# Kernel optimization log

Measured on AMD Instinct MI355X. Metric: run time of the kernel, lower is better.

Reference implementation:

```python
import jax, jax.numpy as jnp
import numpy as np

B, N, K = 4, 1024, 20
DM, DI, DS, DC, DR = 1024, 2048, 16, 4, 64
BITS, GRID = 10, 0.02
BINS = (1, 2, 4, 8, 16, 32)


def _lrelu(x):
    return jnp.where(x >= 0, x, 0.2 * x)


def _bn(x, w, b, m, v, eps=1e-5):
    return (x - m) * (w * jax.lax.rsqrt(v + eps)) + b


def _ln(x, w, b, eps=1e-5):
    mu = jnp.mean(x, -1, keepdims=True)
    var = jnp.mean((x - mu) ** 2, -1, keepdims=True)
    return (x - mu) * jax.lax.rsqrt(var + eps) * w + b


def _knn(x, k):
    # x: (B,N,C) -> (B,N,k) indices of k nearest (largest neg sq dist)
    xx = jnp.sum(x * x, -1)
    d = 2 * jnp.einsum('bnc,bmc->bnm', x, x) - xx[:, :, None] - xx[:, None, :]
    return jax.lax.top_k(d, k)[1]


def _edge_conv(x, w, bw, bb, bm, bv, k):
    idx = _knn(x, k)
    nb = jax.vmap(lambda f, i: f[i])(x, idx)            # (B,N,k,C) row gather
    ctr = jnp.broadcast_to(x[:, :, None, :], nb.shape)
    feat = jnp.concatenate([nb - ctr, ctr], -1)         # (B,N,k,2C)
    h = _lrelu(_bn(jnp.einsum('bnkc,oc->bnko', feat, w), bw, bb, bm, bv))
    return jnp.max(h, axis=2)                           # (B,N,O)


def _hilbert(g):
    # Skilling's AxesToTranspose, 3D, BITS bits/axis. g: (...,3) int32 -> (...,) int32
    xs = [g[..., i] for i in range(3)]
    Q = 1 << (BITS - 1)
    while Q > 1:
        P = Q - 1
        for i in range(3):
            cond = (xs[i] & Q) != 0
            if i == 0:
                xs[0] = jnp.where(cond, xs[0] ^ P, xs[0])
            else:
                t = (xs[0] ^ xs[i]) & P
                n0 = jnp.where(cond, xs[0] ^ P, xs[0] ^ t)
                ni = jnp.where(cond, xs[i], xs[i] ^ t)
                xs[0], xs[i] = n0, ni
        Q >>= 1
    for i in range(1, 3):
        xs[i] = xs[i] ^ xs[i - 1]
    t = jnp.zeros_like(xs[0])
    Q = 1 << (BITS - 1)
    while Q > 1:
        t = jnp.where((xs[2] & Q) != 0, t ^ (Q - 1), t)
        Q >>= 1
    xs = [v ^ t for v in xs]
    code = jnp.zeros_like(xs[0])
    for bit in range(BITS - 1, -1, -1):
        for i in range(3):
            code = (code << 1) | ((xs[i] >> bit) & 1)
    return code


def _serial_order(pts, trans):
    g = jnp.floor(pts / GRID).astype(jnp.int32)
    g = g - jnp.min(g, axis=1, keepdims=True)
    g = jnp.clip(g, 0, (1 << BITS) - 1)
    if trans:
        g = g[..., jnp.array([1, 0, 2])]
    return jnp.argsort(_hilbert(g), axis=1)             # per-batch serialization order


def _take(f, o):
    return jnp.take_along_axis(f, o[..., None], axis=1)


def _mamba(x, in_w, conv_w, conv_b, xproj_w, dt_w, dt_b, A_log, Dp, out_w):
    Bm, L, _ = x.shape
    xc, z = jnp.split(x @ in_w.T, 2, axis=-1)           # (B,L,DI) each
    xp = jnp.pad(xc, ((0, 0), (DC - 1, 0), (0, 0)))     # causal depthwise conv
    xc = sum(conv_w[:, j] * xp[:, j:j + L, :] for j in range(DC)) + conv_b
    xc = jax.nn.silu(xc)
    xdbl = xc @ xproj_w.T
    dt, Bs, Cs = jnp.split(xdbl, [DR, DR + DS], axis=-1)
    dt = jax.nn.softplus(dt @ dt_w.T + dt_b)            # (B,L,DI)
    A = -jnp.exp(A_log)                                 # (DI,DS)

    def step(h, inp):
        dt_t, B_t, C_t, u_t = inp
        h = h * jnp.exp(dt_t[..., None] * A) + (dt_t * u_t)[..., None] * B_t[:, None, :]
        return h, jnp.einsum('bdn,bn->bd', h, C_t)

    tm = lambda a: jnp.moveaxis(a, 1, 0)
    h0 = jnp.zeros((Bm, DI, DS), x.dtype)
    _, ys = jax.lax.scan(step, h0, (tm(dt), tm(Bs), tm(Cs), tm(xc)))
    y = jnp.moveaxis(ys, 0, 1) + xc * Dp
    return (y * jax.nn.silu(z)) @ out_w.T


def _forward(x, c1_w, bn1_w, bn1_b, bn1_m, bn1_v, c2_w, bn2_w, bn2_b, bn2_m, bn2_v,
             c3_w, bn3_w, bn3_b, bn3_m, bn3_v, c4_w, bn4_w, bn4_b, bn4_m, bn4_v,
             c5_w, bn5_w, bn5_b, bn5_m, bn5_v, pe1_w, pe1_b, pe2_w, pe2_b,
             gamma, beta, blkn_w, blkn_b, in_w, conv_w, conv_b, xproj_w,
             dt_w, dt_b, A_log, D, out_w, normf_w, normf_b, ft_w, ft_b):
    pts = jnp.transpose(x, (0, 2, 1))                   # (B,N,3)
    x1 = _edge_conv(pts, c1_w, bn1_w, bn1_b, bn1_m, bn1_v, K)
    x2 = _edge_conv(x1, c2_w, bn2_w, bn2_b, bn2_m, bn2_v, K)
    x3 = _edge_conv(x2, c3_w, bn3_w, bn3_b, bn3_m, bn3_v, K)
    x4 = _edge_conv(x3, c4_w, bn4_w, bn4_b, bn4_m, bn4_v, K)
    dg = _lrelu(_bn(jnp.einsum('bnc,oc->bno', jnp.concatenate([x1, x2, x3, x4], -1), c5_w),
                    bn5_w, bn5_b, bn5_m, bn5_v))        # (B,N,1024)
    pos5 = jax.nn.gelu(pts @ pe1_w.T + pe1_b, approximate=False) @ pe2_w.T + pe2_b
    of = _serial_order(pts, False)
    ob = _serial_order(pts, True)
    xs = jnp.concatenate([_take(dg, of) * gamma + beta,
                          _take(dg, ob) * gamma + beta], 1)   # (B,2N,1024)
    ps = jnp.concatenate([_take(pos5, of), _take(pos5, ob)], 1)
    hs = xs + ps
    hs = hs + _mamba(_ln(hs, blkn_w, blkn_b), in_w, conv_w, conv_b, xproj_w,
                     dt_w, dt_b, A_log, D, out_w)
    hs = _ln(hs, normf_w, normf_b)
    x_all = jnp.concatenate([hs, dg], axis=1)           # (B,3N,1024)
    P = x_all.shape[1]
    feats = []
    for nbin in BINS:
        zz = x_all.reshape(B, nbin, P // nbin, DM)
        feats.append(jnp.mean(zz, 2) + jnp.max(zz, 2))
    bf = jnp.transpose(jnp.concatenate(feats, 1), (1, 0, 2))  # (63,B,1024)
    return bf @ ft_w.T + ft_b                           # (63,B,256)


def setup_inputs() -> dict:
    ks = iter(jax.random.split(jax.random.key(0), 80))
    f32 = jnp.float32
    def nrm(shape, s):
        return jax.random.normal(next(ks), shape, f32) * s
    d = {}
    d['x'] = jax.random.normal(next(ks), (B, 3, N), f32)
    for name, (o, i) in dict(c1=(64, 6), c2=(64, 128), c3=(128, 128),
                             c4=(256, 256), c5=(1024, 512)).items():
        d[name + '_w'] = nrm((o, i), 1.0 / np.sqrt(i))
    for name, c in dict(bn1=64, bn2=64, bn3=128, bn4=256, bn5=1024).items():
        d[name + '_w'] = 1.0 + nrm((c,), 0.05)
        d[name + '_b'] = nrm((c,), 0.05)
        d[name + '_m'] = nrm((c,), 0.05)
        d[name + '_v'] = 1.0 + 0.1 * jax.random.uniform(next(ks), (c,), f32)
    d['pe1_w'] = nrm((DM // 2, 3), 1.0 / np.sqrt(3))
    d['pe1_b'] = nrm((DM // 2,), 0.02)
    d['pe2_w'] = nrm((DM, DM // 2), 1.0 / np.sqrt(DM // 2))
    d['pe2_b'] = nrm((DM,), 0.02)
    d['gamma'] = 1.0 + nrm((DM,), 0.02)
    d['beta'] = nrm((DM,), 0.02)
    d['blkn_w'] = jnp.ones((DM,), f32)
    d['blkn_b'] = jnp.zeros((DM,), f32)
    d['in_w'] = nrm((2 * DI, DM), 1.0 / np.sqrt(DM))
    d['conv_w'] = nrm((DI, DC), 1.0 / np.sqrt(DC))
    d['conv_b'] = jnp.zeros((DI,), f32)
    d['xproj_w'] = nrm((DR + 2 * DS, DI), 1.0 / np.sqrt(DI))
    d['dt_w'] = nrm((DI, DR), DR ** -0.5)
    dt = jnp.exp(jax.random.uniform(next(ks), (DI,), f32) * np.log(0.1 / 1e-3) + np.log(1e-3))
    d['dt_b'] = dt + jnp.log(-jnp.expm1(-dt))           # inverse softplus
    d['A_log'] = jnp.log(jnp.broadcast_to(jnp.arange(1, DS + 1, dtype=f32), (DI, DS)))
    d['D'] = jnp.ones((DI,), f32)
    d['out_w'] = nrm((DM, DI), 1.0 / np.sqrt(DI))
    d['normf_w'] = jnp.ones((DM,), f32)
    d['normf_b'] = jnp.zeros((DM,), f32)
    d['ft_w'] = nrm((256, DM), 1.0 / np.sqrt(DM))
    d['ft_b'] = jnp.zeros((256,), f32)
    return d


def reference(x, c1_w, bn1_w, bn1_b, bn1_m, bn1_v, c2_w, bn2_w, bn2_b, bn2_m, bn2_v,
              c3_w, bn3_w, bn3_b, bn3_m, bn3_v, c4_w, bn4_w, bn4_b, bn4_m, bn4_v,
              c5_w, bn5_w, bn5_b, bn5_m, bn5_v, pe1_w, pe1_b, pe2_w, pe2_b,
              gamma, beta, blkn_w, blkn_b, in_w, conv_w, conv_b, xproj_w,
              dt_w, dt_b, A_log, D, out_w, normf_w, normf_b, ft_w, ft_b):
    return _forward(x, c1_w, bn1_w, bn1_b, bn1_m, bn1_v, c2_w, bn2_w, bn2_b, bn2_m, bn2_v,
                    c3_w, bn3_w, bn3_b, bn3_m, bn3_v, c4_w, bn4_w, bn4_b, bn4_m, bn4_v,
                    c5_w, bn5_w, bn5_b, bn5_m, bn5_v, pe1_w, pe1_b, pe2_w, pe2_b,
                    gamma, beta, blkn_w, blkn_b, in_w, conv_w, conv_b, xproj_w,
                    dt_w, dt_b, A_log, D, out_w, normf_w, normf_b, ft_w, ft_b)
```

## Files before the change

kernel.cpp:

```cpp
#include <hip/hip_runtime.h>
#include <hip/hip_bf16.h>
#include <cstdint>
#include <cstddef>

static constexpr int BB = 4, NN = 1024;
static constexpr int DM = 1024, DI = 2048, DSN = 16, DCN = 4;
static constexpr int LL = 2048, PP = 3072;

typedef unsigned short u16;
typedef __bf16 bfv8 __attribute__((ext_vector_type(8)));
typedef float fv4 __attribute__((ext_vector_type(4)));

__device__ __forceinline__ u16 f2bf(float f) {
  unsigned u = __float_as_uint(f);
  return (u16)((u + 0x7FFFu + ((u >> 16) & 1u)) >> 16);
}
__device__ __forceinline__ float bf2f(u16 h) { return __uint_as_float(((unsigned)h) << 16); }

__device__ __forceinline__ void gload_lds16(const void* g, void* l) {
  __builtin_amdgcn_global_load_lds((const __attribute__((address_space(1))) void*)g,
                                   (__attribute__((address_space(3))) void*)l, 16, 0, 0);
}

__global__ __launch_bounds__(256) void k_fill(unsigned* __restrict__ p, unsigned n32, unsigned pat) {
// ... 93 lines not shown
#pragma unroll
    for (int kk = 0; kk < 16; ++kk) {
      float a[4], bv[4];
#pragma unroll
      for (int i = 0; i < 4; ++i) a[i] = As[kk][(trow << 2) + i];
#pragma unroll
      for (int j = 0; j < 4; ++j) bv[j] = Bs[kk][(tcol << 2) + j];
#pragma unroll
      for (int i = 0; i < 4; ++i)
#pragma unroll
        for (int j = 0; j < 4; ++j) acc[i][j] += a[i] * bv[j];
    }
    __syncthreads();
  }

#pragma unroll
  for (int i = 0; i < 4; ++i) {
    int gm = m0 + (trow << 2) + i;
#pragma unroll
    for (int j = 0; j < 4; ++j) {
      int gn = n0 + (tcol << 2) + j;
      float v = 2.f * acc[i][j] - xx[(b << 10) + gm] - xx[(b << 10) + gn];
      D[((size_t)(b << 10) + gm) * 1024 + gn] = v;
    }
  }
}

__global__ __launch_bounds__(256) void k_sel(const float* __restrict__ D, int* __restrict__ idxo) {
  const int wv = threadIdx.x >> 6, lane = threadIdx.x & 63;
  const int row = (blockIdx.x << 2) + wv;
  const float* dr = D + (size_t)row * 1024;
  float4 c0 = *(const float4*)(dr + (lane << 2));
  float4 c1 = *(const float4*)(dr + 256 + (lane << 2));
  float4 c2 = *(const float4*)(dr + 512 + (lane << 2));
  float4 c3 = *(const float4*)(dr + 768 + (lane << 2));
  float v[16] = {c0.x, c0.y, c0.z, c0.w, c1.x, c1.y, c1.z, c1.w,
                 c2.x, c2.y, c2.z, c2.w, c3.x, c3.y, c3.z, c3.w};
  const int gbase = lane << 2;
  for (int t = 0; t < 20; ++t) {
    float bv = v[0];
    int bi = gbase;
#pragma unroll
    for (int r = 1; r < 16; ++r) {
      int gi = ((r >> 2) << 8) + gbase + (r & 3);
      if (v[r] > bv) { bv = v[r]; bi = gi; }
    }
#pragma unroll
    for (int o = 32; o; o >>= 1) {
      float ov = __shfl_down(bv, o);
      int oi = __shfl_down(bi, o);
      if (ov > bv || (ov == bv && oi < bi)) { bv = ov; bi = oi; }
    }
    bi = __shfl(bi, 0);
    if (lane == 0) idxo[row * 20 + t] = bi;
#pragma unroll
    for (int r = 0; r < 16; ++r) {
      int gi = ((r >> 2) << 8) + gbase + (r & 3);
      if (gi == bi) v[r] = -3e38f;
    }
  }
}

template <int O>
__global__ __launch_bounds__(256) void k_edge_max(const float* __restrict__ G, const float* __restrict__ base,
                                                  const int* __restrict__ idxi,
                                                  const float* __restrict__ bw, const float* __restrict__ bbp,
                                                  const float* __restrict__ bm, const float* __restrict__ bvv,
                                                  float* __restrict__ out, int ldo) {
  __shared__ int ids[20];
  const int rn = blockIdx.x;
  const int tid = threadIdx.x;
  if (tid < 20) ids[tid] = idxi[rn * 20 + tid];
  __syncthreads();
  const int b = rn >> 10;
  float mx = -3e38f, mn = 3e38f;
#pragma unroll 5
  for (int k = 0; k < 20; ++k) {
    float v = G[((size_t)(b << 10) + ids[k]) * O + tid];
    mx = fmaxf(mx, v); mn = fminf(mn, v);
  }
  float s = bw[tid] * rsqrtf(bvv[tid] + 1e-5f);
  float red = (s >= 0.f) ? mx : mn;
  float v = (base[(size_t)rn * O + tid] + red - bm[tid]) * s + bbp[tid];
  out[(size_t)rn * ldo + tid] = (v >= 0.f) ? v : 0.2f * v;
}

template <int EPI>
__global__ __launch_bounds__(256) void k_gemm(const float* __restrict__ A, int lda,
                                              const float* __restrict__ Bm, int ldb, int boff, int bdiff,
                                              float* __restrict__ C, int ldc, int M, int N, int Kd,
                                              const float* __restrict__ p1) {
  __shared__ float As[16][68];
  __shared__ float Bs[16][68];
  const int tid = threadIdx.x;
  const int m0 = blockIdx.y << 6, n0 = blockIdx.x << 6;
  const int tcol = tid & 15, trow = tid >> 4;
  float acc[4][4];
#pragma unroll
  for (int i = 0; i < 4; ++i)
#pragma unroll
    for (int j = 0; j < 4; ++j) acc[i][j] = 0.f;

  for (int k0 = 0; k0 < Kd; k0 += 16) {
#pragma unroll
    for (int p = 0; p < 4; ++p) {
      int lin = tid + (p << 8);
      int r = lin >> 4, kk = lin & 15;
      int gk = k0 + kk;
      int gm = m0 + r;
      As[kk][r] = (gm < M && gk < Kd) ? A[(size_t)gm * lda + gk] : 0.f;
      int gn = n0 + r;
      float bv = 0.f;
      if (gn < N && gk < Kd) {
        bv = Bm[(size_t)gn * ldb + gk + boff];
        if (bdiff) bv -= Bm[(size_t)gn * ldb + gk];
      }
      Bs[kk][r] = bv;
    }
    __syncthreads();
#pragma unroll
    for (int kk = 0; kk < 16; ++kk) {
      float a[4], bv[4];
#pragma unroll
      for (int i = 0; i < 4; ++i) a[i] = As[kk][(trow << 2) + i];
#pragma unroll
      for (int j = 0; j < 4; ++j) bv[j] = Bs[kk][(tcol << 2) + j];
#pragma unroll
      for (int i = 0; i < 4; ++i)
#pragma unroll
        for (int j = 0; j < 4; ++j) acc[i][j] += a[i] * bv[j];
    }
    __syncthreads();
  }

#pragma unroll
  for (int i = 0; i < 4; ++i) {
    int gm = m0 + (trow << 2) + i;
    if (gm >= M) continue;
#pragma unroll
    for (int j = 0; j < 4; ++j) {
      int gn = n0 + (tcol << 2) + j;
      if (gn >= N) continue;
      float v = acc[i][j];
      if (EPI == 2) {
        v += p1[gn];
        v = 0.5f * v * (1.f + erff(v * 0.70710678118654752440f));
      }
      C[(size_t)gm * ldc + gn] = v;
    }
  }
}

template <int EPI>
__global__ __launch_bounds__(256) void k_mgemm(const u16* __restrict__ A, const u16* __restrict__ W,
                                               float* __restrict__ C, int ldc, int M, int N, int K, int alda,
                                               const float* __restrict__ p1, const float* __restrict__ p2,
                                               const float* __restrict__ p3, const float* __restrict__ p4,
                                               u16* __restrict__ obf, void* outp, const void* modesrc) {
  __shared__ u16 Asl[2][4096];
  __shared__ u16 Bsl[2][4096];
  const int tid = threadIdx.x;
  const int lane = tid & 63, wave = tid >> 6;
  const int wm = wave & 1, wn = wave >> 1;
  const int m0 = blockIdx.y << 7, n0 = blockIdx.x << 7;
  fv4 acc[4][4];
#pragma unroll
  for (int i = 0; i < 4; ++i)
#pragma unroll
    for (int j = 0; j < 4; ++j) acc[i][j] = fv4{0.f, 0.f, 0.f, 0.f};

  const int lrow = tid >> 2;
  const int lcol = (((tid & 3) ^ ((tid >> 3) & 3)) << 3);
  const u16* gA0 = A + (size_t)(m0 + lrow) * alda + lcol;
  const u16* gA1 = A + (size_t)(m0 + 64 + lrow) * alda + lcol;
  const u16* gB0 = W + (size_t)(n0 + lrow) * K + lcol;
  const u16* gB1 = W + (size_t)(n0 + 64 + lrow) * K + lcol;
  const int ar = wm * 64 + (lane & 15);
  const int br = wn * 64 + (lane & 15);
  const int swz = ((lane & 15) >> 1) & 3;
  const int ko = (((lane >> 4) ^ swz) << 3);

  gload_lds16(gA0, &Asl[0][wave * 512]);
  gload_lds16(gA1, &Asl[0][2048 + wave * 512]);
  gload_lds16(gB0, &Bsl[0][wave * 512]);
  gload_lds16(gB1, &Bsl[0][2048 + wave * 512]);
  __syncthreads();

  int cur = 0;
  for (int k0 = 0; k0 < K; k0 += 32) {
    if (k0 + 32 < K) {
      const int nb = cur ^ 1;
      gload_lds16(gA0 + k0 + 32, &Asl[nb][wave * 512]);
      gload_lds16(gA1 + k0 + 32, &Asl[nb][2048 + wave * 512]);
      gload_lds16(gB0 + k0 + 32, &Bsl[nb][wave * 512]);
      gload_lds16(gB1 + k0 + 32, &Bsl[nb][2048 + wave * 512]);
    }
    bfv8 af[4], bfr[4];
#pragma unroll
    for (int f = 0; f < 4; ++f) {
      af[f]  = *(const bfv8*)(&Asl[cur][(ar + f * 16) * 32 + ko]);
      bfr[f] = *(const bfv8*)(&Bsl[cur][(br + f * 16) * 32 + ko]);
    }
#pragma unroll
    for (int i = 0; i < 4; ++i)
#pragma unroll
      for (int j = 0; j < 4; ++j)
        acc[i][j] = __builtin_amdgcn_mfma_f32_16x16x32_bf16(af[i], bfr[j], acc[i][j], 0, 0, 0);
    __syncthreads();
    cur ^= 1;
  }

  const int rq = lane >> 4, cq = lane & 15;
#pragma unroll
  for (int i = 0; i < 4; ++i) {
#pragma unroll
    for (int j = 0; j < 4; ++j) {
#pragma unroll
      for (int r = 0; r < 4; ++r) {
        int gm = m0 + wm * 64 + i * 16 + rq * 4 + r;
        int gn = n0 + wn * 64 + j * 16 + cq;
        if (gm >= M || gn >= N) continue;
        float v = acc[i][j][r];
        if (EPI == 1) {
          float s = p1[gn] * rsqrtf(p4[gn] + 1e-5f);
          v = (v - p3[gn]) * s + p2[gn];
          v = (v >= 0.f) ? v : 0.2f * v;
          obf[(size_t)gm * ldc + gn] = f2bf(v);
        } else if (EPI == 3) {
          C[(size_t)gm * ldc + gn] = v + p1[gn];
        } else if (EPI == 5) {
          C[(size_t)gm * ldc + gn] += v;
        } else if (EPI == 6) {
          v += p1[gn];
          bool isbf = (*(const unsigned*)modesrc) != 0x3F800000u;
          if (isbf) ((u16*)outp)[(size_t)gm * ldc + gn] = f2bf(v);
          else ((float*)outp)[(size_t)gm * ldc + gn] = v;
        } else if (EPI == 8) {
          obf[(size_t)gm * ldc + gn] = f2bf(v);
        } else if (EPI == 9) {
          v += p1[gn];
          v = (v > 0.f) ? v + log1pf(expf(-v)) : log1pf(expf(v));
          obf[(size_t)gm * ldc + gn] = f2bf(v);
        } else {
          C[(size_t)gm * ldc + gn] = v;
        }
      }
    }
  }
}

__device__ __forceinline__ int hilbert3(int x0, int x1, int x2) {
  for (int Q = 1 << 9; Q > 1; Q >>= 1) {
    int P2 = Q - 1;
    if (x0 & Q) x0 ^= P2;
    { int t = (x0 ^ x1) & P2; if (x1 & Q) x0 ^= P2; else { x0 ^= t; x1 ^= t; } }
    { int t = (x0 ^ x2) & P2; if (x2 & Q) x0 ^= P2; else { x0 ^= t; x2 ^= t; } }
  }
  x1 ^= x0; x2 ^= x1;
  int t = 0;
  for (int Q = 1 << 9; Q > 1; Q >>= 1)
    if (x2 & Q) t ^= (Q - 1);
  x0 ^= t; x1 ^= t; x2 ^= t;
  int code = 0;
  for (int bit = 9; bit >= 0; --bit) {
    code = (code << 1) | ((x0 >> bit) & 1);
    code = (code << 1) | ((x1 >> bit) & 1);
    code = (code << 1) | ((x2 >> bit) & 1);
  }
  return code;
}

__global__ __launch_bounds__(1024) void k_serial(const float* __restrict__ pts, int* __restrict__ of, int* __restrict__ ob) {
  const int b = blockIdx.x >> 1, trans = blockIdx.x & 1;
  const int tid = threadIdx.x;
  __shared__ int mn[3];
  __shared__ unsigned long long sk[1024];
  if (tid < 3) mn[tid] = 0x7fffffff;
  __syncthreads();
  int g[3];
#pragma unroll
  for (int c = 0; c < 3; ++c) {
    float p = pts[((size_t)b * NN + tid) * 3 + c];
    g[c] = (int)floorf(p / 0.02f);
    atomicMin(&mn[c], g[c]);
  }
  __syncthreads();
#pragma unroll
  for (int c = 0; c < 3; ++c) {
    g[c] -= mn[c];
    g[c] = g[c] < 0 ? 0 : (g[c] > 1023 ? 1023 : g[c]);
  }
  int x0 = g[0], x1 = g[1], x2 = g[2];
  if (trans) { int t = x0; x0 = x1; x1 = t; }
  int code = hilbert3(x0, x1, x2);
  sk[tid] = ((unsigned long long)(unsigned)code << 10) | (unsigned)tid;
  __syncthreads();
  for (int k2 = 2; k2 <= 1024; k2 <<= 1) {
    for (int j = k2 >> 1; j > 0; j >>= 1) {
      int ixj = tid ^ j;
      if (ixj > tid) {
        unsigned long long a0 = sk[tid], a1 = sk[ixj];
        bool up = ((tid & k2) == 0);
        if ((a0 > a1) == up) { sk[tid] = a1; sk[ixj] = a0; }
      }
      __syncthreads();
    }
  }
  int* dst = trans ? ob : of;
  dst[b * NN + tid] = (int)(sk[tid] & 1023u);
}

__global__ __launch_bounds__(256) void k_build_hs(const u16* __restrict__ dg, const float* __restrict__ pos5,
                                                  const int* __restrict__ of, const int* __restrict__ ob,
                                                  const float* __restrict__ gamma, const float* __restrict__ beta,
                                                  float* __restrict__ hs) {
  const int row = blockIdx.x;
  const int b = row >> 11, l = row & 2047;
  const int src = (l < NN) ? of[b * NN + l] : ob[b * NN + (l - NN)];
  const u16* dgr = dg + ((size_t)b * NN + src) * DM;
  const float* psr = pos5 + ((size_t)b * NN + src) * DM;
  float* hr = hs + (size_t)row * DM;
  for (int c = threadIdx.x; c < DM; c += 256)
    hr[c] = bf2f(dgr[c]) * gamma[c] + beta[c] + psr[c];
}

__device__ __forceinline__ float wred_sum(float s) {
#pragma unroll
  for (int o = 32; o; o >>= 1) s += __shfl_down(s, o);
  return s;
}

template <int BF>
__global__ __launch_bounds__(256) void k_ln(const float* X, const float* __restrict__ w,
                                            const float* __restrict__ bb, float* Y, u16* Ybf) {
  const int row = blockIdx.x;
  const float* x = X + (size_t)row * DM;
  const int tid = threadIdx.x;
  float v[4];
#pragma unroll
  for (int p = 0; p < 4; ++p) v[p] = x[tid + (p << 8)];
  __shared__ float red[4];
  float s = ((v[0] + v[1]) + (v[2] + v[3]));
  s = wred_sum(s);
  if ((tid & 63) == 0) red[tid >> 6] = s;
  __syncthreads();
  float mu = (red[0] + red[1] + red[2] + red[3]) * (1.f / DM);
  __syncthreads();
  float ss = 0.f;
#pragma unroll
  for (int p = 0; p < 4; ++p) { float d = v[p] - mu; ss += d * d; }
  ss = wred_sum(ss);
  if ((tid & 63) == 0) red[tid >> 6] = ss;
  __syncthreads();
  float var = (red[0] + red[1] + red[2] + red[3]) * (1.f / DM);
  float rs = rsqrtf(var + 1e-5f);
#pragma unroll
  for (int p = 0; p < 4; ++p) {
    int c = tid + (p << 8);
    float o = (v[p] - mu) * rs * w[c] + bb[c];
    if (BF) Ybf[(size_t)row * DM + c] = f2bf(o);
    else Y[(size_t)row * DM + c] = o;
  }
}

__global__ __launch_bounds__(512) void k_convip(float* __restrict__ x, const float* __restrict__ cw,
                                                const float* __restrict__ cb, u16* __restrict__ xbf) {
  const int b = blockIdx.x >> 5, dgp = blockIdx.x & 31;
  const int lane = threadIdx.x & 63, ch = threadIdx.x >> 6;
  const int d = (dgp << 6) + lane;
  float* base = x + ((size_t)b * LL) * DI + d;
  u16* bb16 = xbf + ((size_t)b * LL) * DI + d;
  const int CL = LL / 8;
  const int l0 = ch * CL;
  const float w0 = cw[d * 4], w1 = cw[d * 4 + 1], w2 = cw[d * 4 + 2], w3 = cw[d * 4 + 3];
  const float bbv = cb[d];
  float a = 0.f, e = 0.f, c = 0.f;
  if (ch) {
    a = base[(size_t)(l0 - 3) * DI];
    e = base[(size_t)(l0 - 2) * DI];
    c = base[(size_t)(l0 - 1) * DI];
  }
  __syncthreads();
  for (int l = l0; l < l0 + CL; ++l) {
    float cur = base[(size_t)l * DI];
    float acc = bbv + w0 * a + w1 * e + w2 * c + w3 * cur;
    a = e; e = c; c = cur;
    float o = acc / (1.f + expf(-acc));
    base[(size_t)l * DI] = o;
    bb16[(size_t)l * DI] = f2bf(o);
  }
}

__global__ __launch_bounds__(64) void k_scanA_f(float* __restrict__ xy, const float* __restrict__ xdbl,
                                                const float* __restrict__ dtw, const float* __restrict__ dtbv,
                                                const float* __restrict__ A_log, const float* __restrict__ Dp,
                                                float* __restrict__ hend, float* __restrict__ dts,
                                                u16* __restrict__ zone) {
  const int t = threadIdx.x;
  const int seg = blockIdx.x & 15;
  const int dgrp = (blockIdx.x >> 4) & 31;
  const int b = blockIdx.x >> 9;
// ... 400 lines not shown
  }
  int o = ((b << 5) + chunk) * 1024 + c;
  psum[o] = sm; pmax[o] = mx;
}

__global__ __launch_bounds__(256) void k_binpool2(const float* __restrict__ psum, const float* __restrict__ pmax,
                                                  float* __restrict__ bf) {
  const int sb = blockIdx.x;
  const int s = sb >> 2, b = sb & 3;
  int nbin, j;
  if (s == 0) { nbin = 1; j = 0; }
  else if (s < 3) { nbin = 2; j = s - 1; }
  else if (s < 7) { nbin = 4; j = s - 3; }
  else if (s < 15) { nbin = 8; j = s - 7; }
  else if (s < 31) { nbin = 16; j = s - 15; }
  else { nbin = 32; j = s - 31; }
  const int nch = 32 / nbin, c0 = j * nch;
  const int tid = threadIdx.x;
#pragma unroll
  for (int p = 0; p < 4; ++p) {
    int c = tid + (p << 8);
    float sm = 0.f, mx = -3e38f;
    for (int k = 0; k < nch; ++k) {
      int idx = ((b << 5) + c0 + k) * 1024 + c;
      sm += psum[idx]; mx = fmaxf(mx, pmax[idx]);
    }
    bf[(size_t)sb * 1024 + c] = sm / (float)(nch * 96) + mx;
  }
}

extern "C" void kernel_launch(void* const* d_in, const int* in_sizes, int n_in,
                              void* d_out, int out_size, void* d_ws, size_t ws_size,
                              hipStream_t stream) {
  const unsigned n32 = (unsigned)(out_size / 2);
  if (n_in != 47) {
    k_fill<<<(n32 + 255) / 256, 256, 0, stream>>>((unsigned*)d_out, n32, 0x44FA44FAu);
    return;
  }
  float* ws = (float*)d_ws;

  unsigned inoff[47];
  unsigned cum = 0;
  for (int i = 0; i < 47; ++i) { inoff[i] = cum; cum += (unsigned)((in_sizes[i] + 63) & ~63); }

  size_t off = ((size_t)cum + 255) & ~(size_t)255;
  auto alloc = [&](size_t nf) { size_t o = off; off = (off + nf + 255) & ~(size_t)255; return o; };
  const size_t O_DG = alloc(2097152);
  const size_t O_HS = alloc(8388608);
  const size_t O_B1 = alloc(16777216);
  const size_t O_B2 = alloc(6291456);
  const size_t O_B3 = alloc(12353536);
  const size_t base_end = off;
  const size_t O_DT = alloc(8388608);
  const size_t dt_end = off;
  if (base_end * 4 > ws_size) {
    k_fill<<<(n32 + 255) / 256, 256, 0, stream>>>((unsigned*)d_out, n32, 0x447A447Au);
    return;
  }
  const bool bigws = (dt_end * 4 <= ws_size);

  auto F = [&](int i) { return ws + inoff[i]; };
  u16*   dg_bf = (u16*)(ws + O_DG);
  float* hs = ws + O_HS;
  float* B1 = ws + O_B1;
  float* B2 = ws + O_B2;
  float* B3 = ws + O_B3;
  u16*   dtb_bf = (u16*)(ws + O_DT);

  float* pts   = B1;
  float* xxb   = B1 + 16384;
  int*   idxb  = (int*)(B1 + 32768);
  int*   of    = (int*)(B1 + 114688);
  int*   ob    = (int*)(B1 + 118784);
  float* xcat  = B1 + 131072;
  float* G     = B1 + 2228224;
  float* baseb = B1 + 3276800;
  float* tb    = B1 + 4325376;
  float* pos5  = B1 + 6422528;
  float* dist  = B1 + 10616832;
  u16*   xcat_bf = (u16*)(B1 + 12582912);
  u16*   tb_bf   = (u16*)(B1 + 14680064);
  float* xyg = B1;
  u16*   lnh_bf = (u16*)B2;
  float* hend   = B2;
  float* hstart = B2 + 2097152;
  float* xdbl   = B2 + 4194304;
  float* bfb    = B2 + 4980736;
  u16*   bfb_bf = (u16*)(B2 + 5238784);
  float* psum   = B2 + 5369856;
  float* pmax   = B2 + 5500928;
  u16*   xdbl_bf = (u16*)(B2 + 5632000);
  float* dtsum  = psum;
  u16* in_w_bf  = (u16*)B3;
  u16* out_w_bf = (u16*)(B3 + 2097152);
  u16* c5_bf    = (u16*)(B3 + 3145728);
  u16* pe2_bf   = (u16*)(B3 + 3407872);
  u16* ft_bf    = (u16*)(B3 + 3670016);
  u16* xpw_bf   = (u16*)(B3 + 3801088);
  u16* dtw_bf   = (u16*)(B3 + 3899392);
  u16* zone     = (u16*)(B3 + 3964928);

  CvtArgs ca;
  unsigned cb = 0;
  for (int i = 0; i < 47; ++i) {
    ca.src[i] = d_in[i];
    ca.dstoff[i] = inoff[i];
    ca.nelem[i] = (unsigned)in_sizes[i];
    ca.cumblk[i] = cb;
    cb += (unsigned)((in_sizes[i] + 1023) / 1024);
  }
  ca.cumblk[47] = cb;
  k_convert<<<cb, 256, 0, stream>>>(ca, ws);

  k_tobf<<<4096, 256, 0, stream>>>(F(34), in_w_bf, 1048576);
  k_tobf<<<2048, 256, 0, stream>>>(F(42), out_w_bf, 524288);
  k_tobf<<<512, 256, 0, stream>>>(F(5), c5_bf, 131072);
  k_tobf<<<512, 256, 0, stream>>>(F(28), pe2_bf, 131072);
  k_tobf<<<256, 256, 0, stream>>>(F(45), ft_bf, 65536);
  k_tobf<<<192, 256, 0, stream>>>(F(37), xpw_bf, 49152);
  k_tobf<<<128, 256, 0, stream>>>(F(38), dtw_bf, 32768);

  k_transpose<<<(BB * NN * 3 + 255) / 256, 256, 0, stream>>>(F(0), pts);

  k_rownorm<<<16, 256, 0, stream>>>(pts, 3, 3, xxb);
  k_dist<<<dim3(16, 16, 4), 256, 0, stream>>>(pts, 3, 3, xxb, dist);
  k_sel<<<1024, 256, 0, stream>>>(dist, idxb);
  k_gemm<0><<<dim3(1, 64), 256, 0, stream>>>(pts, 3, F(1), 6, 0, 0, G, 64, 4096, 64, 3, nullptr);
  k_gemm<0><<<dim3(1, 64), 256, 0, stream>>>(pts, 3, F(1), 6, 3, 1, baseb, 64, 4096, 64, 3, nullptr);
  k_edge_max<64><<<4096, 64, 0, stream>>>(G, baseb, idxb, F(6), F(7), F(8), F(9), xcat + 0, 512);

  k_rownorm<<<16, 256, 0, stream>>>(xcat, 512, 64, xxb);
  k_dist<<<dim3(16, 16, 4), 256, 0, stream>>>(xcat, 512, 64, xxb, dist);
  k_sel<<<1024, 256, 0, stream>>>(dist, idxb);
  k_gemm<0><<<dim3(1, 64), 256, 0, stream>>>(xcat, 512, F(2), 128, 0, 0, G, 64, 4096, 64, 64, nullptr);
  k_gemm<0><<<dim3(1, 64), 256, 0, stream>>>(xcat, 512, F(2), 128, 64, 1, baseb, 64, 4096, 64, 64, nullptr);
  k_edge_max<64><<<4096, 64, 0, stream>>>(G, baseb, idxb, F(10), F(11), F(12), F(13), xcat + 64, 512);

  k_rownorm<<<16, 256, 0, stream>>>(xcat + 64, 512, 64, xxb);
  k_dist<<<dim3(16, 16, 4), 256, 0, stream>>>(xcat + 64, 512, 64, xxb, dist);
  k_sel<<<1024, 256, 0, stream>>>(dist, idxb);
  k_gemm<0><<<dim3(2, 64), 256, 0, stream>>>(xcat + 64, 512, F(3), 128, 0, 0, G, 128, 4096, 128, 64, nullptr);
  k_gemm<0><<<dim3(2, 64), 256, 0, stream>>>(xcat + 64, 512, F(3), 128, 64, 1, baseb, 128, 4096, 128, 64, nullptr);
  k_edge_max<128><<<4096, 128, 0, stream>>>(G, baseb, idxb, F(14), F(15), F(16), F(17), xcat + 128, 512);

  k_rownorm<<<16, 256, 0, stream>>>(xcat + 128, 512, 128, xxb);
  k_dist<<<dim3(16, 16, 4), 256, 0, stream>>>(xcat + 128, 512, 128, xxb, dist);
  k_sel<<<1024, 256, 0, stream>>>(dist, idxb);
  k_gemm<0><<<dim3(4, 64), 256, 0, stream>>>(xcat + 128, 512, F(4), 256, 0, 0, G, 256, 4096, 256, 128, nullptr);
  k_gemm<0><<<dim3(4, 64), 256, 0, stream>>>(xcat + 128, 512, F(4), 256, 128, 1, baseb, 256, 4096, 256, 128, nullptr);
  k_edge_max<256><<<4096, 256, 0, stream>>>(G, baseb, idxb, F(18), F(19), F(20), F(21), xcat + 256, 512);

  const float* np = nullptr;
  k_tobf<<<2048, 256, 0, stream>>>(xcat, xcat_bf, 524288);
  k_mgemm<1><<<dim3(8, 32), 256, 0, stream>>>(xcat_bf, c5_bf, nullptr, 1024, 4096, 1024, 512, 512,
                                              F(22), F(23), F(24), F(25), dg_bf, nullptr, nullptr);

  k_gemm<2><<<dim3(8, 64), 256, 0, stream>>>(pts, 3, F(26), 3, 0, 0, tb, 512, 4096, 512, 3, F(27));
  k_tobf<<<2048, 256, 0, stream>>>(tb, tb_bf, 524288);
  k_mgemm<3><<<dim3(8, 32), 256, 0, stream>>>(tb_bf, pe2_bf, pos5, 1024, 4096, 1024, 512, 512,
                                              F(29), np, np, np, nullptr, nullptr, nullptr);

  k_serial<<<8, 1024, 0, stream>>>(pts, of, ob);

  k_build_hs<<<8192, 256, 0, stream>>>(dg_bf, pos5, of, ob, F(30), F(31), hs);

  k_ln<1><<<8192, 256, 0, stream>>>(hs, F(32), F(33), nullptr, lnh_bf);
  k_mgemm<0><<<dim3(16, 64), 256, 0, stream>>>(lnh_bf, in_w_bf, xyg, 2048, 8192, 2048, 1024, 1024,
                                               np, np, np, np, nullptr, nullptr, nullptr);
  k_convip<<<128, 512, 0, stream>>>(xyg, F(35), F(36), zone);
  k_mgemm<0><<<dim3(1, 64), 256, 0, stream>>>(zone, xpw_bf, xdbl, 96, 8192, 96, 2048, 2048,
                                              np, np, np, np, nullptr, nullptr, nullptr);
  if (bigws) {
    k_tobf<<<768, 256, 0, stream>>>(xdbl, xdbl_bf, 196608);
    k_mgemm<9><<<dim3(16, 64), 256, 0, stream>>>(xdbl_bf, dtw_bf, nullptr, 2048, 8192, 2048, 64, 96,
                                                 F(39), np, np, np, dtb_bf, nullptr, nullptr);
  }
  k_mgemm<8><<<dim3(16, 64), 256, 0, stream>>>(lnh_bf, in_w_bf + 2097152, nullptr, 2048, 8192, 2048, 1024, 1024,
                                               np, np, np, np, zone, nullptr, nullptr);
  if (bigws) {
    k_scanA_p<<<2048, 64, 0, stream>>>(xyg, xdbl, dtb_bf, F(40), F(41), hend, dtsum, zone);
    k_scanB<<<32, 256, 0, stream>>>(hend, dtsum, F(40), hstart);
    k_scanC_p<<<1920, 64, 0, stream>>>(xyg, xdbl, dtb_bf, F(40), hstart, zone);
  } else {
    k_scanA_f<<<2048, 64, 0, stream>>>(xyg, xdbl, F(38), F(39), F(40), F(41), hend, dtsum, zone);
    k_scanB<<<32, 256, 0, stream>>>(hend, dtsum, F(40), hstart);
    k_scanC_f<<<1920, 64, 0, stream>>>(xyg, xdbl, F(38), F(39), F(40), hstart, zone);
  }
  k_mgemm<5><<<dim3(8, 64), 256, 0, stream>>>(zone, out_w_bf, hs, 1024, 8192, 1024, 2048, 2048,
                                              np, np, np, np, nullptr, nullptr, nullptr);

  k_ln<0><<<8192, 256, 0, stream>>>(hs, F(43), F(44), hs, nullptr);

  k_binpool1<<<512, 256, 0, stream>>>(hs, dg_bf, psum, pmax);
  k_binpool2<<<252, 256, 0, stream>>>(psum, pmax, bfb);

  k_tobf<<<252, 256, 0, stream>>>(bfb, bfb_bf, 64512);
  k_mgemm<6><<<dim3(2, 2), 256, 0, stream>>>(bfb_bf, ft_bf, nullptr, 256, 252, 256, 1024, 1024,
                                             F(46), np, np, np, nullptr, d_out, d_in[32]);
}
```

Before: 1.447 ms.

## Add 4-stage LDS-ring MFMA GEMM with prefetch depth two and one barrier

Adds k_mgemm3, a bf16 MFMA GEMM that uses a four-slot LDS ring. It prefetches two K-tiles ahead and waits with explicit vmcnt counts, so each iteration needs one barrier instead of two syncthreads. Most large GEMM launches switch to it, aiming to hide global-load latency better. LDS use doubles to 64KB per block, which may lower occupancy, and the ring-slot reuse relies on the single barrier ordering correctly.

```diff
diff --git a/kernel.cpp b/kernel.cpp
--- a/kernel.cpp
+++ b/kernel.cpp
@@ -269,64 +269,10 @@
 }
 
 template <int EPI>
-__global__ __launch_bounds__(256) void k_mgemm(const u16* __restrict__ A, const u16* __restrict__ W,
-                                               float* __restrict__ C, int ldc, int M, int N, int K, int alda,
-                                               const float* __restrict__ p1, const float* __restrict__ p2,
-                                               const float* __restrict__ p3, const float* __restrict__ p4,
-                                               u16* __restrict__ obf, void* outp, const void* modesrc) {
-  __shared__ u16 Asl[2][4096];
-  __shared__ u16 Bsl[2][4096];
-  const int tid = threadIdx.x;
-  const int lane = tid & 63, wave = tid >> 6;
-  const int wm = wave & 1, wn = wave >> 1;
-  const int m0 = blockIdx.y << 7, n0 = blockIdx.x << 7;
-  fv4 acc[4][4];
-#pragma unroll
-  for (int i = 0; i < 4; ++i)
-#pragma unroll
-    for (int j = 0; j < 4; ++j) acc[i][j] = fv4{0.f, 0.f, 0.f, 0.f};
-
-  const int lrow = tid >> 2;
-  const int lcol = (((tid & 3) ^ ((tid >> 3) & 3)) << 3);
-  const u16* gA0 = A + (size_t)(m0 + lrow) * alda + lcol;
-  const u16* gA1 = A + (size_t)(m0 + 64 + lrow) * alda + lcol;
-  const u16* gB0 = W + (size_t)(n0 + lrow) * K + lcol;
-  const u16* gB1 = W + (size_t)(n0 + 64 + lrow) * K + lcol;
-  const int ar = wm * 64 + (lane & 15);
-  const int br = wn * 64 + (lane & 15);
-  const int swz = ((lane & 15) >> 1) & 3;
-  const int ko = (((lane >> 4) ^ swz) << 3);
-
-  gload_lds16(gA0, &Asl[0][wave * 512]);
-  gload_lds16(gA1, &Asl[0][2048 + wave * 512]);
-  gload_lds16(gB0, &Bsl[0][wave * 512]);
-  gload_lds16(gB1, &Bsl[0][2048 + wave * 512]);
-  __syncthreads();
-
-  int cur = 0;
-  for (int k0 = 0; k0 < K; k0 += 32) {
-    if (k0 + 32 < K) {
-      const int nb = cur ^ 1;
-      gload_lds16(gA0 + k0 + 32, &Asl[nb][wave * 512]);
-      gload_lds16(gA1 + k0 + 32, &Asl[nb][2048 + wave * 512]);
-      gload_lds16(gB0 + k0 + 32, &Bsl[nb][wave * 512]);
-      gload_lds16(gB1 + k0 + 32, &Bsl[nb][2048 + wave * 512]);
-    }
-    bfv8 af[4], bfr[4];
-#pragma unroll
-    for (int f = 0; f < 4; ++f) {
-      af[f]  = *(const bfv8*)(&Asl[cur][(ar + f * 16) * 32 + ko]);
-      bfr[f] = *(const bfv8*)(&Bsl[cur][(br + f * 16) * 32 + ko]);
-    }
-#pragma unroll
-    for (int i = 0; i < 4; ++i)
-#pragma unroll
-      for (int j = 0; j < 4; ++j)
-        acc[i][j] = __builtin_amdgcn_mfma_f32_16x16x32_bf16(af[i], bfr[j], acc[i][j], 0, 0, 0);
-    __syncthreads();
-    cur ^= 1;
-  }
-
+__device__ __forceinline__ void mg_epilogue(fv4 (&acc)[4][4], int lane, int wm, int wn, int m0, int n0,
+                                            float* C, int ldc, int M, int N,
+                                            const float* p1, const float* p2, const float* p3, const float* p4,
+                                            u16* obf, void* outp, const void* modesrc) {
   const int rq = lane >> 4, cq = lane & 15;
 #pragma unroll
   for (int i = 0; i < 4; ++i) {
@@ -364,6 +310,138 @@
       }
     }
   }
+}
+
+template <int EPI>
+__global__ __launch_bounds__(256) void k_mgemm(const u16* __restrict__ A, const u16* __restrict__ W,
+                                               float* __restrict__ C, int ldc, int M, int N, int K, int alda,
+                                               const float* __restrict__ p1, const float* __restrict__ p2,
+                                               const float* __restrict__ p3, const float* __restrict__ p4,
+                                               u16* __restrict__ obf, void* outp, const void* modesrc) {
+  __shared__ u16 Asl[2][4096];
+  __shared__ u16 Bsl[2][4096];
+  const int tid = threadIdx.x;
+  const int lane = tid & 63, wave = tid >> 6;
+  const int wm = wave & 1, wn = wave >> 1;
+  const int m0 = blockIdx.y << 7, n0 = blockIdx.x << 7;
+  fv4 acc[4][4];
+#pragma unroll
+  for (int i = 0; i < 4; ++i)
+#pragma unroll
+    for (int j = 0; j < 4; ++j) acc[i][j] = fv4{0.f, 0.f, 0.f, 0.f};
+
+  const int lrow = tid >> 2;
+  const int lcol = (((tid & 3) ^ ((tid >> 3) & 3)) << 3);
+  const u16* gA0 = A + (size_t)(m0 + lrow) * alda + lcol;
+  const u16* gA1 = A + (size_t)(m0 + 64 + lrow) * alda + lcol;
+  const u16* gB0 = W + (size_t)(n0 + lrow) * K + lcol;
+  const u16* gB1 = W + (size_t)(n0 + 64 + lrow) * K + lcol;
+  const int ar = wm * 64 + (lane & 15);
+  const int br = wn * 64 + (lane & 15);
+  const int swz = ((lane & 15) >> 1) & 3;
+  const int ko = (((lane >> 4) ^ swz) << 3);
+
+  gload_lds16(gA0, &Asl[0][wave * 512]);
+  gload_lds16(gA1, &Asl[0][2048 + wave * 512]);
+  gload_lds16(gB0, &Bsl[0][wave * 512]);
+  gload_lds16(gB1, &Bsl[0][2048 + wave * 512]);
+  __syncthreads();
+
+  int cur = 0;
+  for (int k0 = 0; k0 < K; k0 += 32) {
+    if (k0 + 32 < K) {
+      const int nb = cur ^ 1;
+      gload_lds16(gA0 + k0 + 32, &Asl[nb][wave * 512]);
+      gload_lds16(gA1 + k0 + 32, &Asl[nb][2048 + wave * 512]);
+      gload_lds16(gB0 + k0 + 32, &Bsl[nb][wave * 512]);
+      gload_lds16(gB1 + k0 + 32, &Bsl[nb][2048 + wave * 512]);
+    }
+    bfv8 af[4], bfr[4];
+#pragma unroll
+    for (int f = 0; f < 4; ++f) {
+      af[f]  = *(const bfv8*)(&Asl[cur][(ar + f * 16) * 32 + ko]);
+      bfr[f] = *(const bfv8*)(&Bsl[cur][(br + f * 16) * 32 + ko]);
+    }
+#pragma unroll
+    for (int i = 0; i < 4; ++i)
+#pragma unroll
+      for (int j = 0; j < 4; ++j)
+        acc[i][j] = __builtin_amdgcn_mfma_f32_16x16x32_bf16(af[i], bfr[j], acc[i][j], 0, 0, 0);
+    __syncthreads();
+    cur ^= 1;
+  }
+  mg_epilogue<EPI>(acc, lane, wm, wn, m0, n0, C, ldc, M, N, p1, p2, p3, p4, obf, outp, modesrc);
+}
+
+template <int EPI>
+__global__ __launch_bounds__(256) void k_mgemm3(const u16* __restrict__ A, const u16* __restrict__ W,
+                                                float* __restrict__ C, int ldc, int M, int N, int K, int alda,
+                                                const float* __restrict__ p1, const float* __restrict__ p2,
+                                                const float* __restrict__ p3, const float* __restrict__ p4,
+                                                u16* __restrict__ obf, void* outp, const void* modesrc) {
+  __shared__ u16 Asl[4][4096];
+  __shared__ u16 Bsl[4][4096];
+  const int tid = threadIdx.x;
+  const int lane = tid & 63, wave = tid >> 6;
+  const int wm = wave & 1, wn = wave >> 1;
+  const int m0 = blockIdx.y << 7, n0 = blockIdx.x << 7;
+  fv4 acc[4][4];
+#pragma unroll
+  for (int i = 0; i < 4; ++i)
+#pragma unroll
+    for (int j = 0; j < 4; ++j) acc[i][j] = fv4{0.f, 0.f, 0.f, 0.f};
+
+  const int lrow = tid >> 2;
+  const int lcol = (((tid & 3) ^ ((tid >> 3) & 3)) << 3);
+  const u16* gA0 = A + (size_t)(m0 + lrow) * alda + lcol;
+  const u16* gA1 = A + (size_t)(m0 + 64 + lrow) * alda + lcol;
+  const u16* gB0 = W + (size_t)(n0 + lrow) * K + lcol;
+  const u16* gB1 = W + (size_t)(n0 + 64 + lrow) * K + lcol;
+  const int ar = wm * 64 + (lane & 15);
+  const int br = wn * 64 + (lane & 15);
+  const int swz = ((lane & 15) >> 1) & 3;
+  const int ko = (((lane >> 4) ^ swz) << 3);
+
+  const int NIT = K >> 5;
+#pragma unroll
+  for (int p = 0; p < 2; ++p) {
+    const int k0 = p << 5;
+    gload_lds16(gA0 + k0, &Asl[p][wave * 512]);
+    gload_lds16(gA1 + k0, &Asl[p][2048 + wave * 512]);
+    gload_lds16(gB0 + k0, &Bsl[p][wave * 512]);
+    gload_lds16(gB1 + k0, &Bsl[p][2048 + wave * 512]);
+  }
+
+  for (int it = 0; it < NIT; ++it) {
+    if (it + 2 < NIT) {
+      const int nb = (it + 2) & 3;
+      const int k0 = (it + 2) << 5;
+      gload_lds16(gA0 + k0, &Asl[nb][wave * 512]);
+      gload_lds16(gA1 + k0, &Asl[nb][2048 + wave * 512]);
+      gload_lds16(gB0 + k0, &Bsl[nb][wave * 512]);
+      gload_lds16(gB1 + k0, &Bsl[nb][2048 + wave * 512]);
+      asm volatile("s_waitcnt vmcnt(8)" ::: "memory");
+    } else if (it + 1 < NIT) {
+      asm volatile("s_waitcnt vmcnt(4)" ::: "memory");
+    } else {
+      asm volatile("s_waitcnt vmcnt(0)" ::: "memory");
+    }
+    __builtin_amdgcn_sched_barrier(0);
+    __builtin_amdgcn_s_barrier();
+    const int cb = it & 3;
+    bfv8 af[4], bfr[4];
+#pragma unroll
+    for (int f = 0; f < 4; ++f) {
+      af[f]  = *(const bfv8*)(&Asl[cb][(ar + f * 16) * 32 + ko]);
+      bfr[f] = *(const bfv8*)(&Bsl[cb][(br + f * 16) * 32 + ko]);
+    }
+#pragma unroll
+    for (int i = 0; i < 4; ++i)
+#pragma unroll
+      for (int j = 0; j < 4; ++j)
+        acc[i][j] = __builtin_amdgcn_mfma_f32_16x16x32_bf16(af[i], bfr[j], acc[i][j], 0, 0, 0);
+  }
+  mg_epilogue<EPI>(acc, lane, wm, wn, m0, n0, C, ldc, M, N, p1, p2, p3, p4, obf, outp, modesrc);
 }
 
 __device__ __forceinline__ int hilbert3(int x0, int x1, int x2) {
@@ -1070,31 +1148,31 @@
 
   const float* np = nullptr;
   k_tobf<<<2048, 256, 0, stream>>>(xcat, xcat_bf, 524288);
-  k_mgemm<1><<<dim3(8, 32), 256, 0, stream>>>(xcat_bf, c5_bf, nullptr, 1024, 4096, 1024, 512, 512,
-                                              F(22), F(23), F(24), F(25), dg_bf, nullptr, nullptr);
+  k_mgemm3<1><<<dim3(8, 32), 256, 0, stream>>>(xcat_bf, c5_bf, nullptr, 1024, 4096, 1024, 512, 512,
+                                               F(22), F(23), F(24), F(25), dg_bf, nullptr, nullptr);
 
   k_gemm<2><<<dim3(8, 64), 256, 0, stream>>>(pts, 3, F(26), 3, 0, 0, tb, 512, 4096, 512, 3, F(27));
   k_tobf<<<2048, 256, 0, stream>>>(tb, tb_bf, 524288);
-  k_mgemm<3><<<dim3(8, 32), 256, 0, stream>>>(tb_bf, pe2_bf, pos5, 1024, 4096, 1024, 512, 512,
-                                              F(29), np, np, np, nullptr, nullptr, nullptr);
+  k_mgemm3<3><<<dim3(8, 32), 256, 0, stream>>>(tb_bf, pe2_bf, pos5, 1024, 4096, 1024, 512, 512,
+                                               F(29), np, np, np, nullptr, nullptr, nullptr);
 
   k_serial<<<8, 1024, 0, stream>>>(pts, of, ob);
 
   k_build_hs<<<8192, 256, 0, stream>>>(dg_bf, pos5, of, ob, F(30), F(31), hs);
 
   k_ln<1><<<8192, 256, 0, stream>>>(hs, F(32), F(33), nullptr, lnh_bf);
-  k_mgemm<0><<<dim3(16, 64), 256, 0, stream>>>(lnh_bf, in_w_bf, xyg, 2048, 8192, 2048, 1024, 1024,
+  k_mgemm3<0><<<dim3(16, 64), 256, 0, stream>>>(lnh_bf, in_w_bf, xyg, 2048, 8192, 2048, 1024, 1024,
+                                                np, np, np, np, nullptr, nullptr, nullptr);
+  k_convip<<<128, 512, 0, stream>>>(xyg, F(35), F(36), zone);
+  k_mgemm3<0><<<dim3(1, 64), 256, 0, stream>>>(zone, xpw_bf, xdbl, 96, 8192, 96, 2048, 2048,
                                                np, np, np, np, nullptr, nullptr, nullptr);
-  k_convip<<<128, 512, 0, stream>>>(xyg, F(35), F(36), zone);
-  k_mgemm<0><<<dim3(1, 64), 256, 0, stream>>>(zone, xpw_bf, xdbl, 96, 8192, 96, 2048, 2048,
-                                              np, np, np, np, nullptr, nullptr, nullptr);
   if (bigws) {
     k_tobf<<<768, 256, 0, stream>>>(xdbl, xdbl_bf, 196608);
     k_mgemm<9><<<dim3(16, 64), 256, 0, stream>>>(xdbl_bf, dtw_bf, nullptr, 2048, 8192, 2048, 64, 96,
                                                  F(39), np, np, np, dtb_bf, nullptr, nullptr);
   }
-  k_mgemm<8><<<dim3(16, 64), 256, 0, stream>>>(lnh_bf, in_w_bf + 2097152, nullptr, 2048, 8192, 2048, 1024, 1024,
-                                               np, np, np, np, zone, nullptr, nullptr);
+  k_mgemm3<8><<<dim3(16, 64), 256, 0, stream>>>(lnh_bf, in_w_bf + 2097152, nullptr, 2048, 8192, 2048, 1024, 1024,
+                                                np, np, np, np, zone, nullptr, nullptr);
   if (bigws) {
     k_scanA_p<<<2048, 64, 0, stream>>>(xyg, xdbl, dtb_bf, F(40), F(41), hend, dtsum, zone);
     k_scanB<<<32, 256, 0, stream>>>(hend, dtsum, F(40), hstart);
@@ -1104,8 +1182,8 @@
     k_scanB<<<32, 256, 0, stream>>>(hend, dtsum, F(40), hstart);
     k_scanC_f<<<1920, 64, 0, stream>>>(xyg, xdbl, F(38), F(39), F(40), hstart, zone);
   }
-  k_mgemm<5><<<dim3(8, 64), 256, 0, stream>>>(zone, out_w_bf, hs, 1024, 8192, 1024, 2048, 2048,
-                                              np, np, np, np, nullptr, nullptr, nullptr);
+  k_mgemm3<5><<<dim3(8, 64), 256, 0, stream>>>(zone, out_w_bf, hs, 1024, 8192, 1024, 2048, 2048,
+                                               np, np, np, np, nullptr, nullptr, nullptr);
 
   k_ln<0><<<8192, 256, 0, stream>>>(hs, F(43), F(44), hs, nullptr);
 
@@ -1113,6 +1191,6 @@
   k_binpool2<<<252, 256, 0, stream>>>(psum, pmax, bfb);
 
   k_tobf<<<252, 256, 0, stream>>>(bfb, bfb_bf, 64512);
-  k_mgemm<6><<<dim3(2, 2), 256, 0, stream>>>(bfb_bf, ft_bf, nullptr, 256, 252, 256, 1024, 1024,
-                                             F(46), np, np, np, nullptr, d_out, d_in[32]);
-}
+  k_mgemm3<6><<<dim3(2, 2), 256, 0, stream>>>(bfb_bf, ft_bf, nullptr, 256, 252, 256, 1024, 1024,
+                                              F(46), np, np, np, nullptr, d_out, d_in[32]);
+}
```

Result: faster. 1.390 ms (-4.0%).
